# Performance work log

Measured on AMD Instinct MI355X. Metric: run time of the kernel, lower is better.

## Reference

```python
import jax, jax.numpy as jnp
import numpy as np

NPOINT, RADIUS, NSAMPLE = 1024, 0.2, 32
EPS = 1e-5


def _fps(xyz, npoint):
    # Iterative farthest point sampling (deterministic start at index 0).
    B, N, _ = xyz.shape
    def step(carry, _):
        distance, farthest = carry
        centroid = jnp.take_along_axis(xyz, farthest[:, None, None], axis=1)  # (B,1,3)
        d = jnp.sum((xyz - centroid) ** 2, -1)                                # (B,N)
        distance = jnp.minimum(distance, d)
        return (distance, jnp.argmax(distance, -1)), farthest
    init = (jnp.full((B, N), 1e10, xyz.dtype), jnp.zeros((B,), jnp.int32))
    _, idx = jax.lax.scan(step, init, None, length=npoint)
    return idx.T  # (B, npoint)


def _gather(points, idx):
    # points (B,N,C), idx (B,S,K) -> (B,S,K,C)
    B, S, K = idx.shape
    flat = jnp.take_along_axis(points, idx.reshape(B, S * K)[:, :, None], axis=1)
    return flat.reshape(B, S, K, points.shape[-1])


def _query_ball(xyz, new_xyz):
    # For each centroid, first NSAMPLE point indices within RADIUS (pad with first hit).
    B, N, _ = xyz.shape
    sqr = jnp.sum((new_xyz[:, :, None, :] - xyz[:, None, :, :]) ** 2, -1)  # (B,S,N)
    gi = jnp.where(sqr > RADIUS ** 2, N, jnp.arange(N, dtype=jnp.int32)[None, None, :])
    gi = jnp.sort(gi, axis=-1)[:, :, :NSAMPLE]
    return jnp.where(gi == N, gi[:, :, :1], gi)  # (B,S,K)


def _cond_layer(x, t_embed, wt, bt, wc, bc, g, b):
    # ConditionalConv1d: x += time_mlp(gelu(t)); 1x1 conv; BatchNorm (batch stats); GELU.
    tp = jax.nn.gelu(t_embed, approximate=False) @ wt.T + bt      # (B,Cin)
    x = x + tp[:, None, None, :]
    y = jnp.einsum('bskc,oc->bsko', x, wc) + bc                   # (B,S,K,Cout)
    mu = jnp.mean(y, axis=(0, 1, 2))
    var = jnp.var(y, axis=(0, 1, 2))
    y = (y - mu) * jax.lax.rsqrt(var + EPS) * g + b
    return jax.nn.gelu(y, approximate=False)


def _forward(xyz, points, t_embed, params):
    fps_idx = _fps(xyz, NPOINT)                                        # (B,S)
    new_xyz = jnp.take_along_axis(xyz, fps_idx[:, :, None], axis=1)    # (B,S,3)
    idx = _query_ball(xyz, new_xyz)                                    # (B,S,K)
    grouped_xyz = _gather(xyz, idx) - new_xyz[:, :, None, :]           # (B,S,K,3)
    grouped_pts = _gather(jnp.swapaxes(points, 1, 2), idx)             # (B,S,K,C)
    x = jnp.concatenate([grouped_xyz, grouped_pts], -1)                # (B,S,K,C+3)
    for p in params:
        x = _cond_layer(x, t_embed, *p)
    new_points = jnp.swapaxes(jnp.max(x, axis=2), 1, 2)                # (B,Cout,S)
    return new_xyz, new_points


def setup_inputs() -> dict:
    key = jax.random.key(0)
    ks = iter(jax.random.split(key, 32))
    B, N, CIN, T = 8, 4096, 64, 128
    chans = [(CIN + 3, 64), (64, 64), (64, 128)]
    inp = {
        "xyz": jax.random.normal(next(ks), (B, N, 3), jnp.float32),
        "points": jax.random.normal(next(ks), (B, CIN, N), jnp.float32),
        "t_embed": jax.random.normal(next(ks), (B, T), jnp.float32),
    }
    for i, (ci, co) in enumerate(chans):
        inp[f"wt{i}"] = jax.random.normal(next(ks), (ci, T), jnp.float32) * 0.05
        inp[f"bt{i}"] = jnp.zeros((ci,), jnp.float32)
        inp[f"wc{i}"] = jax.random.normal(next(ks), (co, ci), jnp.float32) * 0.1
        inp[f"bc{i}"] = jnp.zeros((co,), jnp.float32)
        inp[f"g{i}"] = jnp.ones((co,), jnp.float32)
        inp[f"be{i}"] = jnp.zeros((co,), jnp.float32)
    return inp


def reference(xyz, points, t_embed,
              wt0, bt0, wc0, bc0, g0, be0,
              wt1, bt1, wc1, bc1, g1, be1,
              wt2, bt2, wc2, bc2, g2, be2):
    params = [(wt0, bt0, wc0, bc0, g0, be0),
              (wt1, bt1, wc1, bc1, g1, be1),
              (wt2, bt2, wc2, bc2, g2, be2)]
    return _forward(xyz, points, t_embed, params)
```

## Files before the change

### kernel.cpp

```cpp
#include <hip/hip_runtime.h>
#include <cmath>

#define Bc 8
#define Nc 4096
#define Sc 1024
#define Kc 32
#define Mc (Bc*Sc*Kc)

typedef float v2f __attribute__((ext_vector_type(2)));

__device__ __forceinline__ float gelu_f(float x){
  return 0.5f*x*(1.0f + erff(x*0.70710678f));
}

__device__ __forceinline__ v2f pk_add(v2f a, v2f b){
  v2f d; asm("v_pk_add_f32 %0, %1, %2" : "=v"(d) : "v"(a), "v"(b)); return d;
}
__device__ __forceinline__ v2f pk_mul(v2f a, v2f b){
  v2f d; asm("v_pk_mul_f32 %0, %1, %2" : "=v"(d) : "v"(a), "v"(b)); return d;
}

#define ROR_MAXF(v, n) { int _t = __builtin_amdgcn_update_dpp(__float_as_int(v), __float_as_int(v), 0x120|(n), 0xF, 0xF, false); \
                         v = fmaxf(v, __int_as_float(_t)); }
#define BC15_MAXF(v)   { int _t = __builtin_amdgcn_update_dpp(__float_as_int(v), __float_as_int(v), 0x142, 0xA, 0xF, false); \
                         v = fmaxf(v, __int_as_float(_t)); }
#define BC31_MAXF(v)   { int _t = __builtin_amdgcn_update_dpp(__float_as_int(v), __float_as_int(v), 0x143, 0xC, 0xF, false); \
                         v = fmaxf(v, __int_as_float(_t)); }

#define TK(v_, i_) { const bool _t = ((v_) > Bv) || (((v_) == Bv) && ((i_) < Bi)); \
  Bv = _t ? (v_) : Bv; Bi = _t ? (i_) : Bi; }

__global__ __launch_bounds__(256) void fused_front_kernel(
    const float* __restrict__ xyz, float* __restrict__ new_xyz,
    const float* __restrict__ points, float* __restrict__ pointsT,
    const float* __restrict__ t_embed,
    const float* __restrict__ wt0, const float* __restrict__ bt0,
    const float* __restrict__ wt1, const float* __restrict__ bt1,
    const float* __restrict__ wt2, const float* __restrict__ bt2,
    float* __restrict__ tp)
{
  __shared__ __align__(16) float smem[17424];
  const int bid = blockIdx.x;
  const int tid = threadIdx.x;

  if (bid < 8){
    const int b = bid;
    const int lane = tid & 63;
    const int wv = tid >> 6;
    const float* xb = xyz + b*Nc*3;
    float*    skv   = smem;
    unsigned* ski   = (unsigned*)(smem + 8);
    int*      shist = (int*)(smem + 16);
    float4*   c4    = (float4*)(smem + 1040);

    const int base = tid << 4;
    float4 f[12];
    const float4* src = (const float4*)(xb + base*3);
#pragma unroll
    for (int q=0;q<12;++q) f[q] = src[q];
#define AR(i) ((i)%4==0 ? f[(i)/4].x : (i)%4==1 ? f[(i)/4].y : (i)%4==2 ? f[(i)/4].z : f[(i)/4].w)
    v2f px2[8], py2[8], pz2[8], d2[8];
#pragma unroll
    for (int k=0;k<8;++k){
      px2[k].x = AR(6*k+0); py2[k].x = AR(6*k+1); pz2[k].x = AR(6*k+2);
      px2[k].y = AR(6*k+3); py2[k].y = AR(6*k+4); pz2[k].y = AR(6*k+5);
      c4[base+2*k  ] = make_float4(px2[k].x, py2[k].x, pz2[k].x, 0.f);
      c4[base+2*k+1] = make_float4(px2[k].y, py2[k].y, pz2[k].y, 0.f);
      d2[k].x = 1e10f; d2[k].y = 1e10f;
    }
#undef AR
    __syncthreads();
    int widx = 0;
    for (int it=0; it<Sc; ++it){
      const float4 cc = c4[widx];
      if (tid==0) shist[it] = widx;
      v2f ncx, ncy, ncz;
      ncx.x=-cc.x; ncx.y=-cc.x; ncy.x=-cc.y; ncy.y=-cc.y; ncz.x=-cc.z; ncz.y=-cc.z;
      float bvx=-1.0f, bvy=-1.0f;
#pragma unroll
      for (int k=0;k<8;++k){
        const v2f dx = pk_add(px2[k], ncx);
        const v2f dy = pk_add(py2[k], ncy);
        const v2f dz = pk_add(pz2[k], ncz);
        const v2f dd = pk_add(pk_add(pk_mul(dx,dx), pk_mul(dy,dy)), pk_mul(dz,dz));
        v2f dn;
        dn.x = fminf(d2[k].x, dd.x);
        dn.y = fminf(d2[k].y, dd.y);
        d2[k] = dn;
        bvx = fmaxf(bvx, dn.x);
        bvy = fmaxf(bvy, dn.y);
      }
      const float bv = fmaxf(bvx, bvy);
      unsigned bi_local = 0xFFFFFFFFu;
#pragma unroll
      for (int k=0;k<8;++k){
        const unsigned c0 = (d2[k].x == bv) ? (unsigned)(base + 2*k    ) : 0xFFFFFFFFu;
        const unsigned c1 = (d2[k].y == bv) ? (unsigned)(base + 2*k + 1) : 0xFFFFFFFFu;
        const unsigned cm = (c0 < c1) ? c0 : c1;
        bi_local = (cm < bi_local) ? cm : bi_local;
      }
      float mv = bv;
      ROR_MAXF(mv,1); ROR_MAXF(mv,2); ROR_MAXF(mv,4); ROR_MAXF(mv,8);
      BC15_MAXF(mv); BC31_MAXF(mv);
      mv = __int_as_float(__builtin_amdgcn_readlane(__float_as_int(mv), 63));
      const unsigned long long mk = __ballot(bv == mv);
      const int src_lane = __ffsll(mk) - 1;
      const unsigned bi = (unsigned)__builtin_amdgcn_readlane((int)bi_local, src_lane);
      const int p4 = (it & 1) << 2;
      if (lane==0){ skv[p4+wv] = mv; ski[p4+wv] = bi; }
      __syncthreads();
      const float4 m4 = *reinterpret_cast<const float4*>(&skv[p4]);
      const uint4  i4 = *reinterpret_cast<const uint4*>(&ski[p4]);
      float Bv = m4.x; unsigned Bi = i4.x;
      TK(m4.y, i4.y) TK(m4.z, i4.z) TK(m4.w, i4.w)
      widx = (int)Bi;
    }
    __syncthreads();
    for (int i = tid; i < Sc; i += 256){
      const float4 cc = c4[shist[i]];
      float* o = new_xyz + ((size_t)b*Sc + i)*3;
      o[0]=cc.x; o[1]=cc.y; o[2]=cc.z;
    }
  } else if (bid < 520){
    const int t  = bid - 8;
    const int tb = t >> 6;
    const int n0 = (t & 63) << 6;
    float (*tile)[65] = (float(*)[65])smem;
    const int sub = tid >> 6;
    const int ln  = tid & 63;
#pragma unroll 4
    for (int cp=0; cp<16; ++cp){
      const int c = (cp<<2) + sub;
      tile[c][ln] = points[((size_t)(tb*64+c))*Nc + n0 + ln];
    }
    __syncthreads();
#pragma unroll 4
    for (int np=0; np<16; ++np){
      const int nl = (np<<2) + sub;
      pointsT[((size_t)(tb*Nc + n0 + nl))*64 + ln] = tile[ln][nl];
    }
  } else {
    float* ge = smem;
    for (int i = tid; i < Bc*128; i += 256) ge[i] = gelu_f(t_embed[i]);
    __syncthreads();
    for (int i = tid; i < 3*Bc*68; i += 256){
      const int l = i / (Bc*68);
      const int r = i - l*(Bc*68);
      const int b = r / 68;
      const int c = r - b*68;
      const int ci = (l==0) ? 67 : 64;
      float v = 0.0f;
      if (c < ci){
        const float* wt = (l==0)?wt0:((l==1)?wt1:wt2);
        const float* bt = (l==0)?bt0:((l==1)?bt1:bt2);
        const float* w = wt + c*128;
        const float* g = ge + b*128;
        float acc = 0.0f;
        for (int t2=0;t2<128;++t2) acc = fmaf(g[t2], w[t2], acc);
        v = acc + bt[c];
      }
      tp[i] = v;
    }
  }
}

__global__ __launch_bounds__(256) void ballgather_kernel(const float* __restrict__ xyz,
    const float* __restrict__ new_xyz, const float* __restrict__ pointsT,
    float* __restrict__ X){
  const int g = (blockIdx.x<<2) + (threadIdx.x>>6);
  const int lane = threadIdx.x & 63;
  const int w = threadIdx.x >> 6;
  const int b = g >> 10;
  const float* xb = xyz + b*Nc*3;
  const float cx = new_xyz[g*3+0];
  const float cy = new_xyz[g*3+1];
  const float cz = new_xyz[g*3+2];
  __shared__ int sidx[4][32];
  int total = 0;
  for (int base=0; base<Nc; base+=64){
    const int i = base + lane;
    float dx=__fsub_rn(cx, xb[i*3+0]);
    float dy=__fsub_rn(cy, xb[i*3+1]);
    float dz=__fsub_rn(cz, xb[i*3+2]);
    float sq=__fadd_rn(__fadd_rn(__fmul_rn(dx,dx),__fmul_rn(dy,dy)),__fmul_rn(dz,dz));
    bool hit = !(sq > 0.04f);
    unsigned long long m = __ballot(hit);
    if (hit){
      int pos = total + (int)__popcll(m & ((1ull<<lane)-1ull));
      if (pos < 32) sidx[w][pos] = i;
    }
    total += (int)__popcll(m);
    if (total >= 32) break;
  }
  const int fill = (total < 32) ? total : 32;
  const int first = sidx[w][0];
  if (lane >= fill && lane < 32) sidx[w][lane] = first;
  for (int k=0; k<32; ++k){
    const int pidx = sidx[w][k];
    const float* pt = pointsT + ((size_t)((b<<12)+pidx))*64;
    float* xr = X + (size_t)((g<<5)+k)*68;
    float v;
    if      (lane==0) v = __fsub_rn(xb[pidx*3+0], cx);
    else if (lane==1) v = __fsub_rn(xb[pidx*3+1], cy);
    else if (lane==2) v = __fsub_rn(xb[pidx*3+2], cz);
    else              v = pt[lane-3];
    xr[lane] = v;
    if (lane < 4){
      const int c = 64 + lane;
      xr[c] = (c<67) ? pt[c-3] : 0.0f;
    }
  }
}

template<int NORMIN, int CI_REAL, int CI_PAD, int LDX>
__global__ __launch_bounds__(256) void mm_kernel(const float* X,
    const float* __restrict__ wc, const float* __restrict__ tp,
    const float* __restrict__ sc_in, const float* __restrict__ sh_in,
    float* Y, float* __restrict__ pS, float* __restrict__ pQ, int o_base)
{
  __shared__ __align__(16) float wT[CI_PAD][64];
  __shared__ __align__(16) float tpr[CI_PAD];
  __shared__ __align__(16) float scN[64], shN[64];
  __shared__ float redS[4][64];
  __shared__ float redQ[4][64];
  const int tid = threadIdx.x;
  const int m0 = blockIdx.x << 8;
  const int b  = blockIdx.x >> 7;
  for (int idx = tid; idx < CI_PAD*64; idx += 256){
    int c = idx >> 6, o = idx & 63;
    wT[c][o] = (c < CI_REAL) ? wc[(o_base + o)*CI_REAL + c] : 0.0f;
  }
  if (tid < CI_PAD) tpr[tid] = tp[b*68 + tid];
  if (NORMIN && tid < 64){ scN[tid] = sc_in[tid]; shN[tid] = sh_in[tid]; }
  __syncthreads();
  const int rg = tid >> 2, cg = tid & 3;
  const float* x0 = X + (size_t)(m0 + (rg<<2)) * LDX;
  float4 acc[4][4];
#pragma unroll
  for (int r=0;r<4;++r)
#pragma unroll
    for (int q=0;q<4;++q) acc[r][q] = make_float4(0.f,0.f,0.f,0.f);

  float4 xpf[4];
#pragma unroll
  for (int r=0;r<4;++r) xpf[r] = *reinterpret_cast<const float4*>(x0 + r*LDX);

#pragma unroll 1
  for (int c = 0; c < CI_PAD; c += 4){
    float4 xc[4];
#pragma unroll
    for (int r=0;r<4;++r) xc[r] = xpf[r];
    if (c + 4 < CI_PAD){
#pragma unroll
      for (int r=0;r<4;++r) xpf[r] = *reinterpret_cast<const float4*>(x0 + r*LDX + (c+4));
    }
    const float4 tpv = *reinterpret_cast<const float4*>(&tpr[c]);
    if (NORMIN){
      const float4 sci = *reinterpret_cast<const float4*>(&scN[c]);
      const float4 shi = *reinterpret_cast<const float4*>(&shN[c]);
#pragma unroll
      for (int r=0;r<4;++r){
        xc[r].x = gelu_f(fmaf(xc[r].x, sci.x, shi.x));
        xc[r].y = gelu_f(fmaf(xc[r].y, sci.y, shi.y));
        xc[r].z = gelu_f(fmaf(xc[r].z, sci.z, shi.z));
        xc[r].w = gelu_f(fmaf(xc[r].w, sci.w, shi.w));
      }
    }
    float4 xr[4];
#pragma unroll
    for (int r=0;r<4;++r)
      xr[r] = make_float4(xc[r].x+tpv.x, xc[r].y+tpv.y, xc[r].z+tpv.z, xc[r].w+tpv.w);
#pragma unroll
    for (int cc=0; cc<4; ++cc){
      const float* wrow = &wT[c+cc][cg<<4];
      const float4 w0 = *reinterpret_cast<const float4*>(wrow);
      const float4 w1 = *reinterpret_cast<const float4*>(wrow+4);
      const float4 w2 = *reinterpret_cast<const float4*>(wrow+8);
      const float4 w3 = *reinterpret_cast<const float4*>(wrow+12);
#pragma unroll
      for (int r=0;r<4;++r){
        const float xs = (cc==0)?xr[r].x:((cc==1)?xr[r].y:((cc==2)?xr[r].z:xr[r].w));
        acc[r][0].x = fmaf(xs, w0.x, acc[r][0].x);
        acc[r][0].y = fmaf(xs, w0.y, acc[r][0].y);
        acc[r][0].z = fmaf(xs, w0.z, acc[r][0].z);
        acc[r][0].w = fmaf(xs, w0.w, acc[r][0].w);
        acc[r][1].x = fmaf(xs, w1.x, acc[r][1].x);
        acc[r][1].y = fmaf(xs, w1.y, acc[r][1].y);
        acc[r][1].z = fmaf(xs, w1.z, acc[r][1].z);
        acc[r][1].w = fmaf(xs, w1.w, acc[r][1].w);
        acc[r][2].x = fmaf(xs, w2.x, acc[r][2].x);
        acc[r][2].y = fmaf(xs, w2.y, acc[r][2].y);
        acc[r][2].z = fmaf(xs, w2.z, acc[r][2].z);
        acc[r][2].w = fmaf(xs, w2.w, acc[r][2].w);
        acc[r][3].x = fmaf(xs, w3.x, acc[r][3].x);
        acc[r][3].y = fmaf(xs, w3.y, acc[r][3].y);
        acc[r][3].z = fmaf(xs, w3.z, acc[r][3].z);
        acc[r][3].w = fmaf(xs, w3.w, acc[r][3].w);
      }
    }
  }
#pragma unroll
  for (int r=0;r<4;++r){
    float4* yp = reinterpret_cast<float4*>(Y + (size_t)(m0 + (rg<<2) + r)*64 + (cg<<4));
#pragma unroll
    for (int q=0;q<4;++q) yp[q] = acc[r][q];
  }
  float4 s[4], q2[4];
#pragma unroll
  for (int q=0;q<4;++q){
    float sx=0,sy=0,sz=0,sw=0, qx=0,qy=0,qz=0,qw=0;
#pragma unroll
    for (int r=0;r<4;++r){
      sx+=acc[r][q].x; qx+=acc[r][q].x*acc[r][q].x;
      sy+=acc[r][q].y; qy+=acc[r][q].y*acc[r][q].y;
      sz+=acc[r][q].z; qz+=acc[r][q].z*acc[r][q].z;
      sw+=acc[r][q].w; qw+=acc[r][q].w*acc[r][q].w;
    }
    s[q]=make_float4(sx,sy,sz,sw); q2[q]=make_float4(qx,qy,qz,qw);
  }
  const int lane = tid & 63, wvv = tid >> 6;
#pragma unroll
  for (int off=32; off>=4; off>>=1){
#pragma unroll
    for (int q=0;q<4;++q){
      s[q].x  += __shfl_down(s[q].x,  off);
      s[q].y  += __shfl_down(s[q].y,  off);
      s[q].z  += __shfl_down(s[q].z,  off);
      s[q].w  += __shfl_down(s[q].w,  off);
      q2[q].x += __shfl_down(q2[q].x, off);
      q2[q].y += __shfl_down(q2[q].y, off);
      q2[q].z += __shfl_down(q2[q].z, off);
      q2[q].w += __shfl_down(q2[q].w, off);
    }
  }
  if (lane < 4){
#pragma unroll
    for (int q=0;q<4;++q){
      redS[wvv][lane*16 + q*4 + 0] = s[q].x;
      redS[wvv][lane*16 + q*4 + 1] = s[q].y;
      redS[wvv][lane*16 + q*4 + 2] = s[q].z;
      redS[wvv][lane*16 + q*4 + 3] = s[q].w;
      redQ[wvv][lane*16 + q*4 + 0] = q2[q].x;
      redQ[wvv][lane*16 + q*4 + 1] = q2[q].y;
      redQ[wvv][lane*16 + q*4 + 2] = q2[q].z;
      redQ[wvv][lane*16 + q*4 + 3] = q2[q].w;
    }
  }
  __syncthreads();
  if (tid < 64){
    float a=0.f, bb=0.f;
#pragma unroll
    for (int w2=0; w2<4; ++w2){ a += redS[w2][tid]; bb += redQ[w2][tid]; }
    pS[(blockIdx.x<<6) + tid] = a;
    pQ[(blockIdx.x<<6) + tid] = bb;
  }
}

__global__ __launch_bounds__(256) void finalize_kernel(const float* __restrict__ pS,
    const float* __restrict__ pQ, const float* __restrict__ g, const float* __restrict__ be,
    float* __restrict__ scale, float* __restrict__ shift, int nblk){
  __shared__ float rS[4][64], rQ[4][64];
  const int o = threadIdx.x & 63;
  const int ch = threadIdx.x >> 6;
  const int per = nblk >> 2;
  float s=0.f, q=0.f;
  const int i0 = ch*per;
#pragma unroll 4
  for (int i=0;i<per;++i){
    s += pS[((i0+i)<<6)+o];
    q += pQ[((i0+i)<<6)+o];
  }
  rS[ch][o]=s; rQ[ch][o]=q;
  __syncthreads();
  if (threadIdx.x < 64){
    float ss = rS[0][o]+rS[1][o]+rS[2][o]+rS[3][o];
    float qq = rQ[0][o]+rQ[1][o]+rQ[2][o]+rQ[3][o];
    const float inv_n = 1.0f/(float)Mc;
    const float mu = ss*inv_n;
    const float var = qq*inv_n - mu*mu;
    const float rs = 1.0f/sqrtf(var + 1e-5f);
    const float sc = rs*g[o];
    scale[o] = sc;
    shift[o] = fmaf(-mu, sc, be[o]);
  }
}

__global__ __launch_bounds__(256) void pool_kernel(const float* __restrict__ Y,
    const float* __restrict__ scale, const float* __restrict__ shift,
    float* __restrict__ out, int o_base){
  __shared__ float pool[32][65];
  const int tid = threadIdx.x;
  const int b  = blockIdx.x >> 5;
  const int s0 = (blockIdx.x & 31) << 5;
  const int c  = tid & 63;
  const int sl0 = tid >> 6;
  const float sc = scale[c], sh = shift[c];
  for (int sp=0; sp<8; ++sp){
    const int sl = (sp<<2) + sl0;
    const int s = s0 + sl;
    const float* yp = Y + ((size_t)((b<<10)+s)<<5)*64 + c;
    float mx = -1e30f;
#pragma unroll 4
    for (int k=0;k<32;++k){
      float v = yp[(size_t)(k<<6)];
      v = gelu_f(fmaf(v, sc, sh));
      mx = fmaxf(mx, v);
    }
    pool[sl][c] = mx;
  }
  __syncthreads();
  for (int p=0;p<8;++p){
    const int c2 = (p<<3) + (tid>>5);
    const int sl = tid & 31;
    out[((size_t)((b<<7) + o_base + c2)<<10) + s0 + sl] = pool[sl][c2];
  }
}

extern "C" void kernel_launch(void* const* d_in, const int* in_sizes, int n_in,
                              void* d_out, int out_size, void* d_ws, size_t ws_size,
                              hipStream_t stream){
  const float* xyz     = (const float*)d_in[0];
  const float* points  = (const float*)d_in[1];
  const float* t_embed = (const float*)d_in[2];
  const float* wt0=(const float*)d_in[3],  *bt0=(const float*)d_in[4],  *wc0=(const float*)d_in[5];
  const float* g0 =(const float*)d_in[7],  *be0=(const float*)d_in[8];
  const float* wt1=(const float*)d_in[9],  *bt1=(const float*)d_in[10], *wc1=(const float*)d_in[11];
  const float* g1 =(const float*)d_in[13], *be1=(const float*)d_in[14];
  const float* wt2=(const float*)d_in[15], *bt2=(const float*)d_in[16], *wc2=(const float*)d_in[17];
  const float* g2 =(const float*)d_in[19], *be2=(const float*)d_in[20];

  float* out_xyz = (float*)d_out;
  float* out_pts = (float*)d_out + Bc*Sc*3;

  float* ws       = (float*)d_ws;
  float* tp       = ws + 0;
  float* pointsT  = ws + 2048;
  float* pS1      = ws + 2099200;
  float* pQ1      = ws + 2230272;
  float* X        = ws + 2361344;
  float* Ya       = ws + 20187136;
  float* pS0      = ws + 36964352;
  float* pQ0      = ws + 37095424;
  float* sc0      = ws + 37226496;
  float* sh0      = sc0 + 64;
  float* sc1      = sc0 + 128;
  float* sh1      = sc0 + 192;
  float* sc2      = sc0 + 256;
  float* sh2      = sc0 + 320;
  float* sc3      = sc0 + 384;
  float* sh3      = sc0 + 448;
  float* Yx       = X;

  const int NBLK = Mc/256;

  fused_front_kernel<<<521, 256, 0, stream>>>(xyz, out_xyz, points, pointsT,
      t_embed, wt0,bt0, wt1,bt1, wt2,bt2, tp);
  ballgather_kernel<<<(Bc*Sc)/4, 256, 0, stream>>>(xyz, out_xyz, pointsT, X);

  mm_kernel<0,67,68,68><<<NBLK, 256, 0, stream>>>(X, wc0, tp, nullptr, nullptr, Ya, pS0, pQ0, 0);
  finalize_kernel<<<1, 256, 0, stream>>>(pS0, pQ0, g0, be0, sc0, sh0, NBLK);

  mm_kernel<1,64,64,64><<<NBLK, 256, 0, stream>>>(Ya, wc1, tp + 544, sc0, sh0, Ya, pS0, pQ0, 0);
  finalize_kernel<<<1, 256, 0, stream>>>(pS0, pQ0, g1, be1, sc1, sh1, NBLK);

  mm_kernel<1,64,64,64><<<NBLK, 256, 0, stream>>>(Ya, wc2, tp + 1088, sc1, sh1, Yx, pS0, pQ0, 0);
  mm_kernel<1,64,64,64><<<NBLK, 256, 0, stream>>>(Ya, wc2, tp + 1088, sc1, sh1, Ya, pS1, pQ1, 64);
  finalize_kernel<<<1, 256, 0, stream>>>(pS0, pQ0, g2,    be2,    sc2, sh2, NBLK);
  finalize_kernel<<<1, 256, 0, stream>>>(pS1, pQ1, g2+64, be2+64, sc3, sh3, NBLK);

  pool_kernel<<<Bc*Sc/32, 256, 0, stream>>>(Yx, sc2, sh2, out_pts, 0);
  pool_kernel<<<Bc*Sc/32, 256, 0, stream>>>(Ya, sc3, sh3, out_pts, 64);
}
```

Baseline: 1.270 ms.

## Run farthest point sampling in a single wavefront to drop block barriers

Restricts the FPS block to one 64-lane wavefront that holds 64 points per lane in registers. The per-iteration cross-wave reduction through shared memory and __syncthreads goes away, and centroids are written to global memory directly inside the loop. In exchange each lane does four times more distance work per iteration and needs far more registers, which is why launch bounds now request occupancy 1. The serial 1024-step chain may get shorter per step or longer because of the lower parallelism.

After: 2.328 ms. 83.3% more time.

```diff
diff --git a/kernel.cpp b/kernel.cpp
--- a/kernel.cpp
+++ b/kernel.cpp
@@ -27,10 +27,7 @@
 #define BC31_MAXF(v)   { int _t = __builtin_amdgcn_update_dpp(__float_as_int(v), __float_as_int(v), 0x143, 0xC, 0xF, false); \
                          v = fmaxf(v, __int_as_float(_t)); }
 
-#define TK(v_, i_) { const bool _t = ((v_) > Bv) || (((v_) == Bv) && ((i_) < Bi)); \
-  Bv = _t ? (v_) : Bv; Bi = _t ? (i_) : Bi; }
-
-__global__ __launch_bounds__(256) void fused_front_kernel(
+__global__ __launch_bounds__(256, 1) void fused_front_kernel(
     const float* __restrict__ xyz, float* __restrict__ new_xyz,
     const float* __restrict__ points, float* __restrict__ pointsT,
     const float* __restrict__ t_embed,
@@ -39,46 +36,50 @@
     const float* __restrict__ wt2, const float* __restrict__ bt2,
     float* __restrict__ tp)
 {
-  __shared__ __align__(16) float smem[17424];
+  __shared__ __align__(16) float smem[16384];
   const int bid = blockIdx.x;
   const int tid = threadIdx.x;
 
   if (bid < 8){
+    if (tid >= 64) return;
     const int b = bid;
-    const int lane = tid & 63;
-    const int wv = tid >> 6;
+    const int lane = tid;
     const float* xb = xyz + b*Nc*3;
-    float*    skv   = smem;
-    unsigned* ski   = (unsigned*)(smem + 8);
-    int*      shist = (int*)(smem + 16);
-    float4*   c4    = (float4*)(smem + 1040);
-
-    const int base = tid << 4;
-    float4 f[12];
-    const float4* src = (const float4*)(xb + base*3);
-#pragma unroll
-    for (int q=0;q<12;++q) f[q] = src[q];
-#define AR(i) ((i)%4==0 ? f[(i)/4].x : (i)%4==1 ? f[(i)/4].y : (i)%4==2 ? f[(i)/4].z : f[(i)/4].w)
-    v2f px2[8], py2[8], pz2[8], d2[8];
-#pragma unroll
-    for (int k=0;k<8;++k){
-      px2[k].x = AR(6*k+0); py2[k].x = AR(6*k+1); pz2[k].x = AR(6*k+2);
-      px2[k].y = AR(6*k+3); py2[k].y = AR(6*k+4); pz2[k].y = AR(6*k+5);
-      c4[base+2*k  ] = make_float4(px2[k].x, py2[k].x, pz2[k].x, 0.f);
-      c4[base+2*k+1] = make_float4(px2[k].y, py2[k].y, pz2[k].y, 0.f);
-      d2[k].x = 1e10f; d2[k].y = 1e10f;
-    }
-#undef AR
-    __syncthreads();
-    int widx = 0;
+    float4* c4 = (float4*)smem;
+    const int base = lane << 6;
+
+    v2f px2[32], py2[32], pz2[32], d2[32];
+    const float4* src = (const float4*)(xb + (size_t)base*3);
+#pragma unroll
+    for (int c=0;c<8;++c){
+      const float4 f0=src[6*c+0], f1=src[6*c+1], f2=src[6*c+2];
+      const float4 f3=src[6*c+3], f4=src[6*c+4], f5=src[6*c+5];
+      px2[4*c+0]=(v2f){f0.x,f0.w}; py2[4*c+0]=(v2f){f0.y,f1.x}; pz2[4*c+0]=(v2f){f0.z,f1.y};
+      px2[4*c+1]=(v2f){f1.z,f2.y}; py2[4*c+1]=(v2f){f1.w,f2.z}; pz2[4*c+1]=(v2f){f2.x,f2.w};
+      px2[4*c+2]=(v2f){f3.x,f3.w}; py2[4*c+2]=(v2f){f3.y,f4.x}; pz2[4*c+2]=(v2f){f3.z,f4.y};
+      px2[4*c+3]=(v2f){f4.z,f5.y}; py2[4*c+3]=(v2f){f4.w,f5.z}; pz2[4*c+3]=(v2f){f5.x,f5.w};
+      d2[4*c+0]=(v2f){1e10f,1e10f}; d2[4*c+1]=(v2f){1e10f,1e10f};
+      d2[4*c+2]=(v2f){1e10f,1e10f}; d2[4*c+3]=(v2f){1e10f,1e10f};
+      c4[base+8*c+0]=make_float4(f0.x,f0.y,f0.z,0.f);
+      c4[base+8*c+1]=make_float4(f0.w,f1.x,f1.y,0.f);
+      c4[base+8*c+2]=make_float4(f1.z,f1.w,f2.x,0.f);
+      c4[base+8*c+3]=make_float4(f2.y,f2.z,f2.w,0.f);
+      c4[base+8*c+4]=make_float4(f3.x,f3.y,f3.z,0.f);
+      c4[base+8*c+5]=make_float4(f3.w,f4.x,f4.y,0.f);
+      c4[base+8*c+6]=make_float4(f4.z,f4.w,f5.x,0.f);
+      c4[base+8*c+7]=make_float4(f5.y,f5.z,f5.w,0.f);
+    }
+    float cx = xb[0], cy = xb[1], cz = xb[2];
     for (int it=0; it<Sc; ++it){
-      const float4 cc = c4[widx];
-      if (tid==0) shist[it] = widx;
+      if (lane==0){
+        float* o = new_xyz + ((size_t)b*Sc + it)*3;
+        o[0]=cx; o[1]=cy; o[2]=cz;
+      }
       v2f ncx, ncy, ncz;
-      ncx.x=-cc.x; ncx.y=-cc.x; ncy.x=-cc.y; ncy.y=-cc.y; ncz.x=-cc.z; ncz.y=-cc.z;
-      float bvx=-1.0f, bvy=-1.0f;
-#pragma unroll
-      for (int k=0;k<8;++k){
+      ncx.x=-cx; ncx.y=-cx; ncy.x=-cy; ncy.y=-cy; ncz.x=-cz; ncz.y=-cz;
+      float bv = -1.0f;
+#pragma unroll
+      for (int k=0;k<32;++k){
         const v2f dx = pk_add(px2[k], ncx);
         const v2f dy = pk_add(py2[k], ncy);
         const v2f dz = pk_add(pz2[k], ncz);
@@ -87,39 +88,25 @@
         dn.x = fminf(d2[k].x, dd.x);
         dn.y = fminf(d2[k].y, dd.y);
         d2[k] = dn;
-        bvx = fmaxf(bvx, dn.x);
-        bvy = fmaxf(bvy, dn.y);
-      }
-      const float bv = fmaxf(bvx, bvy);
-      unsigned bi_local = 0xFFFFFFFFu;
-#pragma unroll
-      for (int k=0;k<8;++k){
+        bv = fmaxf(bv, fmaxf(dn.x, dn.y));
+      }
+      unsigned bi = 0xFFFFFFFFu;
+#pragma unroll
+      for (int k=0;k<32;++k){
         const unsigned c0 = (d2[k].x == bv) ? (unsigned)(base + 2*k    ) : 0xFFFFFFFFu;
         const unsigned c1 = (d2[k].y == bv) ? (unsigned)(base + 2*k + 1) : 0xFFFFFFFFu;
         const unsigned cm = (c0 < c1) ? c0 : c1;
-        bi_local = (cm < bi_local) ? cm : bi_local;
+        bi = (cm < bi) ? cm : bi;
       }
       float mv = bv;
       ROR_MAXF(mv,1); ROR_MAXF(mv,2); ROR_MAXF(mv,4); ROR_MAXF(mv,8);
       BC15_MAXF(mv); BC31_MAXF(mv);
       mv = __int_as_float(__builtin_amdgcn_readlane(__float_as_int(mv), 63));
       const unsigned long long mk = __ballot(bv == mv);
-      const int src_lane = __ffsll(mk) - 1;
-      const unsigned bi = (unsigned)__builtin_amdgcn_readlane((int)bi_local, src_lane);
-      const int p4 = (it & 1) << 2;
-      if (lane==0){ skv[p4+wv] = mv; ski[p4+wv] = bi; }
-      __syncthreads();
-      const float4 m4 = *reinterpret_cast<const float4*>(&skv[p4]);
-      const uint4  i4 = *reinterpret_cast<const uint4*>(&ski[p4]);
-      float Bv = m4.x; unsigned Bi = i4.x;
-      TK(m4.y, i4.y) TK(m4.z, i4.z) TK(m4.w, i4.w)
-      widx = (int)Bi;
-    }
-    __syncthreads();
-    for (int i = tid; i < Sc; i += 256){
-      const float4 cc = c4[shist[i]];
-      float* o = new_xyz + ((size_t)b*Sc + i)*3;
-      o[0]=cc.x; o[1]=cc.y; o[2]=cc.z;
+      const int sl = __ffsll(mk) - 1;
+      const unsigned wbi = (unsigned)__builtin_amdgcn_readlane((int)bi, sl);
+      const float4 cc = c4[wbi];
+      cx = cc.x; cy = cc.y; cz = cc.z;
     }
   } else if (bid < 520){
     const int t  = bid - 8;
```
